# Optimization experiments

Measured on AMD Instinct MI355X. Metric: run time of the kernel, lower is better.

## Reference

```python
import jax, jax.numpy as jnp
import numpy as np

KNOWLEDGE_RANK = 128
COARSE_K = 20
FINE_K = 10


def setup_inputs() -> dict:
    key = jax.random.key(0)
    ks = jax.random.split(key, 5)
    B, S, D, N, R = 2, 2048, 1024, 65536, KNOWLEDGE_RANK
    return {
        "x": jax.random.normal(ks[0], (B, S, D), dtype=jnp.float32),
        "W_router": jax.random.normal(ks[1], (D, N), dtype=jnp.float32) * (1.0 / np.sqrt(D)),
        "W_enc": jax.random.normal(ks[2], (D, R), dtype=jnp.float32) * (1.0 / np.sqrt(D)),
        "K_all": jax.random.normal(ks[3], (N, R), dtype=jnp.float32) * 0.02,
        "V_all": jax.random.normal(ks[4], (N, D), dtype=jnp.float32) * 0.02,
    }


def reference(x, W_router, W_enc, K_all, V_all):
    # x: [B,S,D]; router logits over the knowledge table: [B,S,N]
    k_logits = jnp.einsum('bsd,dn->bsn', x, W_router)
    coarse_scores, candidate_idx = jax.lax.top_k(k_logits, COARSE_K)  # [B,S,C]

    query = jnp.einsum('bsd,dr->bsr', x, W_enc)  # [B,S,R]
    K_cand = K_all[candidate_idx]                # [B,S,C,R] irregular gather
    fine_scores = jnp.einsum('bsr,bscr->bsc', query, K_cand) / np.sqrt(KNOWLEDGE_RANK)

    fine_topk_scores, fine_local_idx = jax.lax.top_k(fine_scores, FINE_K)  # [B,S,F]
    fine_weights = jax.nn.softmax(fine_topk_scores, axis=-1)               # [B,S,F]
    fine_global_idx = jnp.take_along_axis(candidate_idx, fine_local_idx, axis=-1)  # [B,S,F]

    selected_V = V_all[fine_global_idx]          # [B,S,F,D] irregular gather
    output = jnp.einsum('bsfd,bsf->bsd', selected_V, fine_weights)
    return output
```

## Files before the change

kernel.cpp:

```cpp
#include <hip/hip_runtime.h>
#include <math.h>
#include <stdint.h>

#define NTOK 4096
#define DIM  1024
#define NCOL 65536
#define RANK 128
#define CK 20
#define FK 10

#define SLABS 16
#define SLABCOLS (NCOL / SLABS)
#define BM 128
#define BN 256
#define BK 32
#define NCHUNK (SLABCOLS / BN)
#define KSTEPS (DIM / BK)
#define CKS 12
#define NPART (SLABS * CKS)
#define POOL 32
#define BUFSZ 24576
#define SELSTRIDE 132

typedef _Float16 f16;
typedef __attribute__((ext_vector_type(8))) _Float16 f16x8;
typedef __attribute__((ext_vector_type(4))) float f32x4;

__device__ __forceinline__ void f32_split(float v, unsigned short& h, unsigned short& l) {
    f16 hh = (f16)v;
    float r = v - (float)hh;
    f16 ll = (f16)r;
    h = __builtin_bit_cast(unsigned short, hh);
    l = __builtin_bit_cast(unsigned short, ll);
}

__device__ __forceinline__ void gll16(const void* src, void* ldsdst) {
    __builtin_amdgcn_global_load_lds(
        (__attribute__((address_space(1))) unsigned int*)src,
        (__attribute__((address_space(3))) unsigned int*)ldsdst, 16, 0, 0);
}

#define WAITVM_(n) asm volatile("s_waitcnt vmcnt(" #n ")" ::: "memory")
#define WAITLGKM0  asm volatile("s_waitcnt lgkmcnt(0)" ::: "memory")

__global__ __launch_bounds__(256)
void k0_convx(const float* __restrict__ x, unsigned short* __restrict__ xh)
{
    int i = blockIdx.x * 256 + threadIdx.x;
    float4 v = ((const float4*)x)[i];
    ushort4 h; unsigned short dummy;
    f32_split(v.x, h.x, dummy); f32_split(v.y, h.y, dummy);
    f32_split(v.z, h.z, dummy); f32_split(v.w, h.w, dummy);
    ((ushort4*)xh)[i] = h;
}

__global__ __launch_bounds__(256)
void k0_convw(const float* __restrict__ W, unsigned short* __restrict__ WhT,
              unsigned short* __restrict__ WlT)
{
    __shared__ float t[64][65];
    const int tid = threadIdx.x;
    const int k0 = blockIdx.x * 64;
    const int n0 = blockIdx.y * 64;
#pragma unroll
    for (int i = 0; i < 16; ++i) {
        int idx = i * 256 + tid;
        int r = idx >> 6, c = idx & 63;
        t[r][c] = W[(size_t)(k0 + r) * NCOL + n0 + c];
    }
    __syncthreads();
#pragma unroll
    for (int i = 0; i < 8; ++i) {
        int idx = i * 256 + tid;
        int n = idx >> 5, kp = idx & 31;
        float a = t[2 * kp][n]     * 1024.0f;
        float b = t[2 * kp + 1][n] * 1024.0f;
        unsigned short ah, al, bh, bl;
        f32_split(a, ah, al);
        f32_split(b, bh, bl);
        unsigned int wh = (unsigned)ah | ((unsigned)bh << 16);
        unsigned int wl = (unsigned)al | ((unsigned)bl << 16);
        size_t row = (size_t)(n0 + n) * DIM + k0;
        *(unsigned int*)(WhT + row + 2 * kp) = wh;
        *(unsigned int*)(WlT + row + 2 * kp) = wl;
    }
}

__global__ __launch_bounds__(512, 4)
void k1_mfma(const unsigned short* __restrict__ xh,
             const unsigned short* __restrict__ WhT,
             float* __restrict__ part_s, int* __restrict__ part_i)
{
    __shared__ __align__(16) unsigned char smem[73728];

    const int tid  = threadIdx.x;
    const int lane = tid & 63;
    const int wave = tid >> 6;
    const int wr = wave >> 2;
    const int wc = wave & 3;
    const int slab = blockIdx.x;
    const int tokbase = blockIdx.y * BM;

    const int srow = wave * 16 + (lane >> 2);
    const int soct = (lane & 3) ^ (srow & 3);
    const unsigned short* pA = xh + (size_t)(tokbase + srow) * DIM + soct * 8;

    const int xorj = (((lane >> 4) ^ (lane & 3)) << 4);
    const int offA0 =        (wr * 64 + (lane & 15)) * 64 + xorj;
    const int offB0 = 8192 + (wc * 64 + (lane & 15)) * 64 + xorj;

    float ts[CKS]; int ti[CKS];
#pragma unroll
    for (int k = 0; k < CKS; ++k) { ts[k] = -INFINITY; ti[k] = 0x7fffffff; }

    float* sel = (float*)smem;

#pragma unroll 1
    for (int nc = 0; nc < NCHUNK; ++nc) {
        const int n0 = slab * SLABCOLS + nc * BN;
        const unsigned short* pB = WhT + (size_t)(n0 + srow) * DIM + soct * 8;

        f32x4 acc[4][4];
        const f32x4 zero = {0.f, 0.f, 0.f, 0.f};
#pragma unroll
        for (int m = 0; m < 4; ++m)
#pragma unroll
            for (int n = 0; n < 4; ++n) acc[m][n] = zero;

        #define STAGE(buf, kk) do {                                             \
            unsigned b_ = (unsigned)(buf) * 24576u + (unsigned)wave * 1024u;    \
            gll16(pA + (size_t)(kk) * BK,                 smem + b_);           \
            gll16(pB + (size_t)(kk) * BK,                 smem + b_ + 8192);    \
            gll16(pB + (size_t)128 * DIM + (kk) * BK,     smem + b_ + 16384);   \
        } while (0)

        STAGE(0, 0);
        STAGE(1, 1);

#pragma unroll 1
        for (int kk = 0; kk < KSTEPS; ++kk) {
            if (kk < KSTEPS - 2) {
                STAGE((kk + 2) % 3, kk + 2);
                WAITVM_(6);
            } else if (kk == KSTEPS - 2) {
                WAITVM_(3);
            } else {
                WAITVM_(0);
            }
            __builtin_amdgcn_s_barrier();

            const unsigned char* bp = smem + (unsigned)(kk % 3) * 24576u;
            f16x8 Af[4];
#pragma unroll
            for (int m = 0; m < 4; ++m) Af[m] = *(const f16x8*)(bp + offA0 + m * 1024);
#pragma unroll
            for (int n = 0; n < 4; ++n) {
                f16x8 Bf = *(const f16x8*)(bp + offB0 + n * 1024);
#pragma unroll
                for (int m = 0; m < 4; ++m)
                    acc[m][n] = __builtin_amdgcn_mfma_f32_16x16x32_f16(Af[m], Bf, acc[m][n], 0, 0, 0);
            }

            WAITLGKM0;
            __builtin_amdgcn_s_barrier();
        }
        #undef STAGE

#pragma unroll 1
        for (int p = 0; p < 2; ++p) {
            if ((wc >> 1) == p) {
                const int colb = (wc & 1) * 64;
#pragma unroll
                for (int m = 0; m < 4; ++m)
#pragma unroll
                    for (int n = 0; n < 4; ++n) {
                        const int col = colb + n * 16 + (lane & 15);
                        const int row = wr * 64 + m * 16 + (lane >> 4) * 4;
#pragma unroll
                        for (int r = 0; r < 4; ++r)
                            sel[(row + r) * SELSTRIDE + col] = acc[m][n][r];
                    }
            }
            __syncthreads();
            {
                const int part = tid & 3;
                const float* rp = sel + (tid >> 2) * SELSTRIDE + part;
                const int ibase = n0 + p * 128 + part;
#pragma unroll 1
                for (int j = 0; j < 32; ++j) {
                    float v = rp[4 * j];
                    if (v > ts[CKS - 1]) {
                        float cv = v; int ci = ibase + 4 * j;
#pragma unroll
                        for (int k = 0; k < CKS; ++k) {
                            bool g = cv > ts[k];
                            float os = ts[k]; int oi = ti[k];
                            ts[k] = g ? cv : os; ti[k] = g ? ci : oi;
                            cv = g ? os : cv;   ci = g ? oi : ci;
                        }
                    }
                }
            }
            __syncthreads();
        }
    }

    float* Ls = (float*)smem;
    int*   Li = (int*)(smem + 24576);
#pragma unroll
    for (int k = 0; k < CKS; ++k) {
        Ls[tid * CKS + k] = ts[k];
        Li[tid * CKS + k] = ti[k];
    }
    __syncthreads();
    if (tid < BM) {
        const int b0 = (tid * 4 + 0) * CKS, b1 = (tid * 4 + 1) * CKS;
        const int b2 = (tid * 4 + 2) * CKS, b3 = (tid * 4 + 3) * CKS;
        int h0 = 0, h1 = 0, h2 = 0, h3 = 0;
        const size_t ob = ((size_t)(tokbase + tid) * SLABS + slab) * CKS;
#pragma unroll 1
        for (int k = 0; k < CKS; ++k) {
            float s0 = Ls[b0 + h0]; int i0 = Li[b0 + h0];
            float s1 = Ls[b1 + h1]; int i1 = Li[b1 + h1];
            float s2 = Ls[b2 + h2]; int i2 = Li[b2 + h2];
            float s3 = Ls[b3 + h3]; int i3 = Li[b3 + h3];
            float bs = s0; int bi = i0; int bp = 0;
            if (s1 > bs || (s1 == bs && i1 < bi)) { bs = s1; bi = i1; bp = 1; }
            if (s2 > bs || (s2 == bs && i2 < bi)) { bs = s2; bi = i2; bp = 2; }
            if (s3 > bs || (s3 == bs && i3 < bi)) { bs = s3; bi = i3; bp = 3; }
            part_s[ob + k] = bs; part_i[ob + k] = bi;
            if      (bp == 0) ++h0;
            else if (bp == 1) ++h1;
            else if (bp == 2) ++h2;
            else              ++h3;
        }
    }
}

__global__ __launch_bounds__(256)
void k3_fine(const float* __restrict__ x, const float* __restrict__ Wenc,
             const float* __restrict__ Kall, const float* __restrict__ Vall,
             const unsigned short* __restrict__ WhT, const unsigned short* __restrict__ WlT,
             const float* __restrict__ part_s, const int* __restrict__ part_i,
             float* __restrict__ out)
{
    const int tok = blockIdx.x;
    const int tid = threadIdx.x;

    __shared__ float xs[DIM];
    __shared__ float qs[RANK];
    __shared__ float ls[NPART];
    __shared__ int   li[NPART];
    __shared__ int   pool[POOL];
    __shared__ float resc[POOL];
    __shared__ int   cand[CK];
    __shared__ float fsc[CK];
    __shared__ float fss[FK];
    __shared__ int   fgi[FK];
    __shared__ float fw[FK];

    ((float4*)xs)[tid] = ((const float4*)(x + (size_t)tok * DIM))[tid];
    if (tid < NPART) {
        ls[tid] = part_s[(size_t)tok * NPART + tid];
        li[tid] = part_i[(size_t)tok * NPART + tid];
    }
    __syncthreads();

    if (tid < NPART) {
        float s = ls[tid]; int idx = li[tid];
        int r = 0;
        for (int e = 0; e < NPART; ++e) {
            float s2 = ls[e]; int i2 = li[e];
            r += (s2 > s) || (s2 == s && i2 < idx);
        }
        if (r < POOL) pool[r] = idx;
    }
    __syncthreads();

    {
        const int c = tid >> 3, oct = tid & 7;
        const int idx = pool[c];
        const ushort4* ph = (const ushort4*)(WhT + (size_t)idx * DIM + oct * 128);
        const ushort4* pl = (const ushort4*)(WlT + (size_t)idx * DIM + oct * 128);
        const float* xp = xs + oct * 128;
        float a = 0.0f;
#pragma unroll 4
        for (int j = 0; j < 32; ++j) {
            ushort4 hv = ph[j], lv = pl[j];
            a = fmaf(xp[j*4+0], (float)__builtin_bit_cast(f16, hv.x) + (float)__builtin_bit_cast(f16, lv.x), a);
            a = fmaf(xp[j*4+1], (float)__builtin_bit_cast(f16, hv.y) + (float)__builtin_bit_cast(f16, lv.y), a);
            a = fmaf(xp[j*4+2], (float)__builtin_bit_cast(f16, hv.z) + (float)__builtin_bit_cast(f16, lv.z), a);
            a = fmaf(xp[j*4+3], (float)__builtin_bit_cast(f16, hv.w) + (float)__builtin_bit_cast(f16, lv.w), a);
        }
        a += __shfl_down(a, 4, 8);
        a += __shfl_down(a, 2, 8);
        a += __shfl_down(a, 1, 8);
        if (oct == 0) resc[c] = a * (1.0f / 1024.0f);
    }
    __syncthreads();

    if (tid < POOL) {
        float s = resc[tid]; int idx = pool[tid];
        int r = 0;
        for (int e = 0; e < POOL; ++e)
            r += (resc[e] > s) || (resc[e] == s && pool[e] < idx);
        if (r < CK) cand[r] = idx;
    }
    __syncthreads();

    if (tid < RANK) {
        float q = 0.0f;
#pragma unroll 8
        for (int d = 0; d < DIM; ++d)
            q = fmaf(xs[d], Wenc[(size_t)d * RANK + tid], q);
        qs[tid] = q;
    }
    __syncthreads();

    if (tid < CK) {
        const float* Kr = Kall + (size_t)cand[tid] * RANK;
        float s = 0.0f;
#pragma unroll 8
        for (int r = 0; r < RANK; ++r) s = fmaf(qs[r], Kr[r], s);
        fsc[tid] = s * 0.08838834764831845f;
    }
    __syncthreads();

    if (tid < CK) {
        float s = fsc[tid]; int r = 0;
        for (int e = 0; e < CK; ++e)
            r += (fsc[e] > s) || (fsc[e] == s && e < tid);
        if (r < FK) { fss[r] = s; fgi[r] = cand[tid]; }
    }
    __syncthreads();

    if (tid == 0) {
        float m = fss[0];
#pragma unroll
        for (int k = 1; k < FK; ++k) m = fmaxf(m, fss[k]);
        float w[FK]; float sum = 0.0f;
#pragma unroll
        for (int k = 0; k < FK; ++k) { w[k] = expf(fss[k] - m); sum += w[k]; }
        float inv = 1.0f / sum;
#pragma unroll
        for (int k = 0; k < FK; ++k) fw[k] = w[k] * inv;
    }
    __syncthreads();

#pragma unroll
    for (int jj = 0; jj < DIM / 256; ++jj) {
        const int d = tid + jj * 256;
        float o = 0.0f;
#pragma unroll
        for (int f = 0; f < FK; ++f)
            o = fmaf(fw[f], Vall[(size_t)fgi[f] * DIM + d], o);
        out[(size_t)tok * DIM + d] = o;
    }
}

__global__ __launch_bounds__(256, 2)
void k1_router_f32(const float* __restrict__ x, const float* __restrict__ Wr,
                   float* __restrict__ part_s, int* __restrict__ part_i)
{
    __shared__ float smem[64][257];
    const int tid     = threadIdx.x;
    const int tokbase = blockIdx.x * 64;
    const int colbase = blockIdx.y * 8192;
    const int mytok   = tid & 63;
    const int mypart  = tid >> 6;

    float ts[CK]; int ti[CK];
#pragma unroll
    for (int k = 0; k < CK; ++k) { ts[k] = -INFINITY; ti[k] = 0x7fffffff; }

#pragma unroll 1
    for (int cg = 0; cg < 32; ++cg) {
        const int n = colbase + cg * 256 + tid;
        float acc[64];
#pragma unroll
        for (int t = 0; t < 64; ++t) acc[t] = 0.0f;
#pragma unroll 1
        for (int dc = 0; dc < DIM; dc += 8) {
            float w[8];
#pragma unroll
            for (int i = 0; i < 8; ++i)
                w[i] = Wr[(size_t)(dc + i) * NCOL + n];
#pragma unroll
            for (int t = 0; t < 64; ++t) {
                const float* xr = x + (size_t)(tokbase + t) * DIM + dc;
#pragma unroll
                for (int i = 0; i < 8; ++i)
                    acc[t] = fmaf(xr[i], w[i], acc[t]);
            }
        }
        __syncthreads();
#pragma unroll
        for (int t = 0; t < 64; ++t) smem[t][tid] = acc[t];
        __syncthreads();
        const int jbase = mypart * 64;
#pragma unroll 1
        for (int j = 0; j < 64; ++j) {
            float v = smem[mytok][jbase + j];
            if (v > ts[CK - 1]) {
                float cv = v; int ci = colbase + cg * 256 + jbase + j;
#pragma unroll
                for (int k = 0; k < CK; ++k) {
                    bool g = cv > ts[k];
                    float os = ts[k]; int oi = ti[k];
                    ts[k] = g ? cv : os; ti[k] = g ? ci : oi;
                    cv = g ? os : cv;   ci = g ? oi : ci;
                }
            }
        }
    }
    __syncthreads();
    float* Ls = &smem[0][0];
    int*   Li = (int*)(Ls + 256 * CK);
#pragma unroll
    for (int k = 0; k < CK; ++k) { Ls[tid * CK + k] = ts[k]; Li[tid * CK + k] = ti[k]; }
    __syncthreads();
    if (tid < 64) {
        const int tok = tid;
        int h0 = 0, h1 = 0, h2 = 0, h3 = 0;
        const size_t ob = ((size_t)(tokbase + tok) * 8 + blockIdx.y) * CK;
#pragma unroll 1
        for (int k = 0; k < CK; ++k) {
            float s0 = Ls[(      tok) * CK + h0]; int i0 = Li[(      tok) * CK + h0];
            float s1 = Ls[( 64 + tok) * CK + h1]; int i1 = Li[( 64 + tok) * CK + h1];
            float s2 = Ls[(128 + tok) * CK + h2]; int i2 = Li[(128 + tok) * CK + h2];
            float s3 = Ls[(192 + tok) * CK + h3]; int i3 = Li[(192 + tok) * CK + h3];
            float bs = s0; int bi = i0; int bp = 0;
            if (s1 > bs || (s1 == bs && i1 < bi)) { bs = s1; bi = i1; bp = 1; }
            if (s2 > bs || (s2 == bs && i2 < bi)) { bs = s2; bi = i2; bp = 2; }
            if (s3 > bs || (s3 == bs && i3 < bi)) { bs = s3; bi = i3; bp = 3; }
            part_s[ob + k] = bs; part_i[ob + k] = bi;
            if      (bp == 0) ++h0;
            else if (bp == 1) ++h1;
            else if (bp == 2) ++h2;
            else              ++h3;
        }
    }
}

template<int CT, int BLK>
__global__ __launch_bounds__(BLK)
void k3_fine_direct(const float* __restrict__ x, const float* __restrict__ Wenc,
                    const float* __restrict__ Kall, const float* __restrict__ Vall,
                    const float* __restrict__ part_s, const int* __restrict__ part_i,
                    float* __restrict__ out)
{
    const int tok = blockIdx.x;
    const int tid = threadIdx.x;

    __shared__ float xs[DIM];
    __shared__ float qs[RANK];
    __shared__ float ls[CT * CK];
    __shared__ int   li[CT * CK];
    __shared__ int   cand[CK];
    __shared__ float fsc[CK];
    __shared__ float fss[FK];
    __shared__ int   fgi[FK];
    __shared__ float fw[FK];

    if (tid < DIM / 4)
        ((float4*)xs)[tid] = ((const float4*)(x + (size_t)tok * DIM))[tid];
    for (int i = tid; i < CT * CK; i += BLK) {
        ls[i] = part_s[(size_t)tok * (CT * CK) + i];
        li[i] = part_i[(size_t)tok * (CT * CK) + i];
    }
    __syncthreads();

    if (tid < CT * CK) {
        float s = ls[tid]; int idx = li[tid];
        int r = 0;
        for (int e = 0; e < CT * CK; ++e) {
            float s2 = ls[e]; int i2 = li[e];
            r += (s2 > s) || (s2 == s && i2 < idx);
        }
        if (r < CK) cand[r] = idx;
    }
    __syncthreads();

    if (tid < RANK) {
        float q = 0.0f;
#pragma unroll 8
        for (int d = 0; d < DIM; ++d)
            q = fmaf(xs[d], Wenc[(size_t)d * RANK + tid], q);
        qs[tid] = q;
    }
    __syncthreads();

    if (tid < CK) {
        const float* Kr = Kall + (size_t)cand[tid] * RANK;
        float s = 0.0f;
#pragma unroll 8
        for (int r = 0; r < RANK; ++r) s = fmaf(qs[r], Kr[r], s);
        fsc[tid] = s * 0.08838834764831845f;
    }
    __syncthreads();

    if (tid < CK) {
        float s = fsc[tid]; int r = 0;
        for (int e = 0; e < CK; ++e)
            r += (fsc[e] > s) || (fsc[e] == s && e < tid);
        if (r < FK) { fss[r] = s; fgi[r] = cand[tid]; }
    }
    __syncthreads();

    if (tid == 0) {
        float m = fss[0];
#pragma unroll
        for (int k = 1; k < FK; ++k) m = fmaxf(m, fss[k]);
        float w[FK]; float sum = 0.0f;
#pragma unroll
        for (int k = 0; k < FK; ++k) { w[k] = expf(fss[k] - m); sum += w[k]; }
        float inv = 1.0f / sum;
#pragma unroll
        for (int k = 0; k < FK; ++k) fw[k] = w[k] * inv;
    }
    __syncthreads();

    for (int d = tid; d < DIM; d += BLK) {
        float o = 0.0f;
#pragma unroll
        for (int f = 0; f < FK; ++f)
            o = fmaf(fw[f], Vall[(size_t)fgi[f] * DIM + d], o);
        out[(size_t)tok * DIM + d] = o;
    }
}

extern "C" void kernel_launch(void* const* d_in, const int* in_sizes, int n_in,
                              void* d_out, int out_size, void* d_ws, size_t ws_size,
                              hipStream_t stream)
{
    (void)in_sizes; (void)n_in; (void)out_size;
    const float* x    = (const float*)d_in[0];
    const float* Wr   = (const float*)d_in[1];
    const float* Wenc = (const float*)d_in[2];
    const float* Kall = (const float*)d_in[3];
    const float* Vall = (const float*)d_in[4];
    float* out = (float*)d_out;

    const size_t off_ps = 0;
    const size_t off_pi = off_ps + (size_t)NTOK * NPART * 4;
    const size_t off_xh = off_pi + (size_t)NTOK * NPART * 4;
    const size_t off_wh = off_xh + (size_t)NTOK * DIM * 2;
    const size_t off_wl = off_wh + (size_t)NCOL * DIM * 2;
    const size_t REQ    = off_wl + (size_t)NCOL * DIM * 2;

    if (ws_size >= REQ) {
        float* part_s = (float*)((char*)d_ws + off_ps);
        int*   part_i = (int*)((char*)d_ws + off_pi);
        unsigned short* xh  = (unsigned short*)((char*)d_ws + off_xh);
        unsigned short* WhT = (unsigned short*)((char*)d_ws + off_wh);
        unsigned short* WlT = (unsigned short*)((char*)d_ws + off_wl);

        k0_convx<<<NTOK * DIM / 1024, 256, 0, stream>>>(x, xh);
        k0_convw<<<dim3(DIM / 64, NCOL / 64), 256, 0, stream>>>(Wr, WhT, WlT);
        k1_mfma<<<dim3(SLABS, NTOK / BM), 512, 0, stream>>>(xh, WhT, part_s, part_i);
        k3_fine<<<NTOK, 256, 0, stream>>>(x, Wenc, Kall, Vall, WhT, WlT, part_s, part_i, out);
    } else {
        float* part_s = (float*)d_ws;
        int*   part_i = (int*)d_ws + (size_t)NTOK * 8 * CK;
        k1_router_f32<<<dim3(NTOK / 64, 8), 256, 0, stream>>>(x, Wr, part_s, part_i);
        k3_fine_direct<8, 256><<<NTOK, 256, 0, stream>>>(x, Wenc, Kall, Vall, part_s, part_i, out);
    }
}
```

Before: 1.277 ms.

## Restructure GEMM pipeline barriers, LDS swizzle, and vectorize top-k scan

Moves the prefetch of stage kk+2 after the per-step barrier so each k-step needs one barrier instead of two, with a single barrier after the loop. It also changes the global-to-LDS row mapping and the XOR swizzle, apparently to cut LDS bank conflicts. The candidate scan now has each thread read contiguous float4 groups with a max prefilter instead of 32 strided scalar loads, which cuts LDS instructions and branch checks. Each thread now scans contiguous column groups rather than interleaved columns, so tie order in the partial lists may differ. With the buffer reuse pattern shortened to a single barrier, a write/read race on the triple buffer is possible.

Measured after the change: 1.687 ms. 32.1% more time.

```diff
diff --git a/kernel.cpp b/kernel.cpp
--- a/kernel.cpp
+++ b/kernel.cpp
@@ -101,19 +101,54 @@
     const int slab = blockIdx.x;
     const int tokbase = blockIdx.y * BM;
 
-    const int srow = wave * 16 + (lane >> 2);
-    const int soct = (lane & 3) ^ (srow & 3);
+    const int srow = tid >> 2;
+    const int soct = (tid & 3) ^ ((tid >> 3) & 3);
     const unsigned short* pA = xh + (size_t)(tokbase + srow) * DIM + soct * 8;
 
-    const int xorj = (((lane >> 4) ^ (lane & 3)) << 4);
-    const int offA0 =        (wr * 64 + (lane & 15)) * 64 + xorj;
-    const int offB0 = 8192 + (wc * 64 + (lane & 15)) * 64 + xorj;
+    const int c4 = lane & 15;
+    const int xj = (((lane >> 4) ^ ((c4 >> 1) & 3)) << 4);
+    const int offA0 =        (wr * 64 + c4) * 64 + xj;
+    const int offB0 = 8192 + (wc * 64 + c4) * 64 + xj;
 
     float ts[CKS]; int ti[CKS];
 #pragma unroll
     for (int k = 0; k < CKS; ++k) { ts[k] = -INFINITY; ti[k] = 0x7fffffff; }
+    const int tok_sel = tid >> 2;
+    const int part    = tid & 3;
 
     float* sel = (float*)smem;
+
+    #define STAGE(pb, buf, kk) do {                                              \
+        unsigned b_ = (unsigned)(buf) * 24576u + (unsigned)wave * 1024u;         \
+        gll16(pA   + (size_t)(kk) * BK,                smem + b_);               \
+        gll16((pb) + (size_t)(kk) * BK,                smem + b_ + 8192);        \
+        gll16((pb) + (size_t)128 * DIM + (kk) * BK,    smem + b_ + 16384);       \
+    } while (0)
+
+    #define SCAN16(ibase_, rp_) do {                                             \
+        _Pragma("unroll")                                                         \
+        for (int j = 0; j < 4; ++j) {                                             \
+            float4 v = *(const float4*)((rp_) + 4 * j);                           \
+            float m01 = fmaxf(v.x, v.y), m23 = fmaxf(v.z, v.w);                   \
+            if (fmaxf(m01, m23) > ts[CKS - 1]) {                                  \
+                float vv[4] = {v.x, v.y, v.z, v.w};                               \
+                _Pragma("unroll")                                                 \
+                for (int e = 0; e < 4; ++e) {                                     \
+                    float cv = vv[e];                                             \
+                    if (cv > ts[CKS - 1]) {                                       \
+                        int ci = (ibase_) + 4 * j + e;                            \
+                        _Pragma("unroll")                                         \
+                        for (int k = 0; k < CKS; ++k) {                           \
+                            bool g = cv > ts[k];                                  \
+                            float os = ts[k]; int oi = ti[k];                     \
+                            ts[k] = g ? cv : os; ti[k] = g ? ci : oi;             \
+                            cv = g ? os : cv;   ci = g ? oi : ci;                 \
+                        }                                                         \
+                    }                                                             \
+                }                                                                 \
+            }                                                                     \
+        }                                                                         \
+    } while (0)
 
 #pragma unroll 1
     for (int nc = 0; nc < NCHUNK; ++nc) {
@@ -127,28 +162,20 @@
 #pragma unroll
             for (int n = 0; n < 4; ++n) acc[m][n] = zero;
 
-        #define STAGE(buf, kk) do {                                             \
-            unsigned b_ = (unsigned)(buf) * 24576u + (unsigned)wave * 1024u;    \
-            gll16(pA + (size_t)(kk) * BK,                 smem + b_);           \
-            gll16(pB + (size_t)(kk) * BK,                 smem + b_ + 8192);    \
-            gll16(pB + (size_t)128 * DIM + (kk) * BK,     smem + b_ + 16384);   \
-        } while (0)
-
-        STAGE(0, 0);
-        STAGE(1, 1);
+        STAGE(pB, 0, 0);
+        STAGE(pB, 1, 1);
 
 #pragma unroll 1
         for (int kk = 0; kk < KSTEPS; ++kk) {
-            if (kk < KSTEPS - 2) {
-                STAGE((kk + 2) % 3, kk + 2);
-                WAITVM_(6);
-            } else if (kk == KSTEPS - 2) {
+            if (kk < KSTEPS - 1) {
                 WAITVM_(3);
             } else {
                 WAITVM_(0);
             }
             __builtin_amdgcn_s_barrier();
 
+            if (kk + 2 < KSTEPS) STAGE(pB, (kk + 2) % 3, kk + 2);
+
             const unsigned char* bp = smem + (unsigned)(kk % 3) * 24576u;
             f16x8 Af[4];
 #pragma unroll
@@ -162,9 +189,8 @@
             }
 
             WAITLGKM0;
-            __builtin_amdgcn_s_barrier();
-        }
-        #undef STAGE
+        }
+        __builtin_amdgcn_s_barrier();
 
 #pragma unroll 1
         for (int p = 0; p < 2; ++p) {
@@ -174,7 +200,7 @@
                 for (int m = 0; m < 4; ++m)
 #pragma unroll
                     for (int n = 0; n < 4; ++n) {
-                        const int col = colb + n * 16 + (lane & 15);
+                        const int col = colb + n * 16 + c4;
                         const int row = wr * 64 + m * 16 + (lane >> 4) * 4;
 #pragma unroll
                         for (int r = 0; r < 4; ++r)
@@ -183,27 +209,14 @@
             }
             __syncthreads();
             {
-                const int part = tid & 3;
-                const float* rp = sel + (tid >> 2) * SELSTRIDE + part;
-                const int ibase = n0 + p * 128 + part;
-#pragma unroll 1
-                for (int j = 0; j < 32; ++j) {
-                    float v = rp[4 * j];
-                    if (v > ts[CKS - 1]) {
-                        float cv = v; int ci = ibase + 4 * j;
-#pragma unroll
-                        for (int k = 0; k < CKS; ++k) {
-                            bool g = cv > ts[k];
-                            float os = ts[k]; int oi = ti[k];
-                            ts[k] = g ? cv : os; ti[k] = g ? ci : oi;
-                            cv = g ? os : cv;   ci = g ? oi : ci;
-                        }
-                    }
-                }
+                const float* rp = sel + tok_sel * SELSTRIDE;
+                SCAN16(n0 + p * 128 +      part * 16, rp +      part * 16);
+                SCAN16(n0 + p * 128 + 64 + part * 16, rp + 64 + part * 16);
             }
             __syncthreads();
         }
     }
+    #undef STAGE
 
     float* Ls = (float*)smem;
     int*   Li = (int*)(smem + 24576);
```
